# Performance work log

Measured on AMD Instinct MI355X. Metric: run time of the kernel, lower is better.

The kernel has to match this reference:

```python
import jax, jax.numpy as jnp
import numpy as np

SCALE = 8
NUM_CLASSES = 15
IGNORE_THRES = 0.5
# anchors for scale=8 divided by scale
GRID_ANCHOR = jnp.array([[96.0 / 8, 230.0 / 8], [79.0 / 8, 186.0 / 8], [81.0 / 8, 133.0 / 8]], dtype=jnp.float32)  # [3,2]


def _bce_sum(p, t, mask):
    # torch BCELoss(reduction='sum') with log clamped at -100, restricted to mask
    lp = jnp.maximum(jnp.log(p), -100.0)
    ln = jnp.maximum(jnp.log(1.0 - p), -100.0)
    return jnp.sum(-(t * lp + (1.0 - t) * ln) * mask)


def setup_inputs() -> dict:
    key = jax.random.key(0)
    k1, k2, k3 = jax.random.split(key, 3)
    nB, nG = 128, 52
    x = jax.random.normal(k1, (nB, 3 * (NUM_CLASSES + 5), nG, nG), dtype=jnp.float32)
    boxes = jax.random.uniform(k2, (nB, 4), minval=0.1, maxval=0.6)  # cx,cy,w,h in (0,1)
    cls = jax.random.randint(k3, (nB, 1), 0, NUM_CLASSES).astype(jnp.float32)
    labels = jnp.concatenate([boxes, cls], axis=-1)  # [nB,5]
    return {"x": x, "labels": labels}


def reference(x, labels):
    nB, nG = x.shape[0], x.shape[2]
    pred = x.reshape(nB, 3, NUM_CLASSES + 5, nG, nG).transpose(0, 1, 3, 4, 2)  # [B,3,G,G,20]
    px = jax.nn.sigmoid(pred[..., 0])
    py = jax.nn.sigmoid(pred[..., 1])
    pw = pred[..., 2]
    ph = pred[..., 3]
    conf = jax.nn.sigmoid(pred[..., 4])
    cls = jax.nn.softmax(pred[..., 5:], axis=-1)
    pred_boxs = jnp.stack([px, py, pw, ph], axis=-1)  # [B,3,G,G,4]
    out = jnp.concatenate([
        pred_boxs.reshape(nB, -1, 4) * SCALE,
        conf.reshape(nB, -1, 1),
        cls.reshape(nB, -1, NUM_CLASSES),
    ], axis=-1)

    # ---- build_targets (vectorized; one target per image as in original loop) ----
    tb = labels[:, :4] * nG  # boxes in grid units [B,4]
    gx, gy, gw, gh = tb[:, 0], tb[:, 1], tb[:, 2], tb[:, 3]
    gi = gx.astype(jnp.int32)
    gj = gy.astype(jnp.int32)
    gcls = labels[:, 4].astype(jnp.int32)

    # wh-IoU anchors vs targets -> [3,B]
    aw, ah = GRID_ANCHOR[:, 0:1], GRID_ANCHOR[:, 1:2]
    inter_wh = jnp.minimum(aw, gw[None, :]) * jnp.minimum(ah, gh[None, :])
    ious = inter_wh / (aw * ah + 1e-16 + gw[None, :] * gh[None, :] - inter_wh)
    best_idx = jnp.argmax(ious, axis=0)  # [B]

    bidx = jnp.arange(nB)
    shape4 = (nB, 3, nG, nG)
    obj = jnp.zeros(shape4, jnp.float32).at[bidx, best_idx, gj, gi].set(1.0)

    noobj = jnp.ones(shape4, jnp.float32)
    arep = jnp.tile(jnp.arange(3), nB)
    brep = jnp.repeat(bidx, 3)
    jrep = jnp.repeat(gj, 3)
    irep = jnp.repeat(gi, 3)
    ign = (jnp.reshape(ious.T, (-1,)) > IGNORE_THRES).astype(jnp.float32)
    noobj = noobj.at[brep, arep, jrep, irep].mul(1.0 - ign)
    noobj = noobj.at[bidx, best_idx, gj, gi].set(0.0)

    gif = gi.astype(jnp.float32)
    gjf = gj.astype(jnp.float32)
    tx = jnp.zeros(shape4, jnp.float32).at[bidx, best_idx, gj, gi].set(gx - gif)
    ty = jnp.zeros(shape4, jnp.float32).at[bidx, best_idx, gj, gi].set(gy - gjf)
    tw = jnp.zeros(shape4, jnp.float32).at[bidx, best_idx, gj, gi].set(jnp.log(gw / GRID_ANCHOR[best_idx, 0] + 1e-16))
    th = jnp.zeros(shape4, jnp.float32).at[bidx, best_idx, gj, gi].set(jnp.log(gh / GRID_ANCHOR[best_idx, 1] + 1e-16))
    tcls = jnp.zeros(shape4 + (NUM_CLASSES,), jnp.float32).at[bidx, best_idx, gj, gi, gcls].set(1.0)

    # cls_mask: does argmax of predicted class at target cell match gt class
    pred_cls_at = cls[bidx, best_idx, gj, gi]  # [B,15]
    cls_hit = (jnp.argmax(pred_cls_at, axis=-1) == gcls).astype(jnp.float32)
    cls_mask = jnp.zeros(shape4, jnp.float32).at[bidx, best_idx, gj, gi].set(cls_hit)

    # iou between pred box at target cell and target box (cxcywh, +1 corner convention)
    pb = pred_boxs[bidx, best_idx, gj, gi]  # [B,4]
    b1x1, b1y1 = pb[:, 0] - pb[:, 2] / 2, pb[:, 1] - pb[:, 3] / 2
    b1x2, b1y2 = pb[:, 0] + pb[:, 2] / 2, pb[:, 1] + pb[:, 3] / 2
    b2x1, b2y1 = gx - gw / 2, gy - gh / 2
    b2x2, b2y2 = gx + gw / 2, gy + gh / 2
    iw = jnp.clip(jnp.minimum(b1x2, b2x2) - jnp.maximum(b1x1, b2x1) + 1, 0)
    ih = jnp.clip(jnp.minimum(b1y2, b2y2) - jnp.maximum(b1y1, b2y1) + 1, 0)
    inter = iw * ih
    a1 = (b1x2 - b1x1 + 1) * (b1y2 - b1y1 + 1)
    a2 = (b2x2 - b2x1 + 1) * (b2y2 - b2y1 + 1)
    iou_vec = inter / (a1 + a2 - inter + 1e-16)
    iou_scores = jnp.zeros(shape4, jnp.float32).at[bidx, best_idx, gj, gi].set(iou_vec)

    tconf = obj
    # ---- losses (boolean-mask indexing replaced by masked sums) ----
    loss_x = jnp.sum(jnp.abs(px - tx) * obj)
    loss_y = jnp.sum(jnp.abs(py - ty) * obj)
    loss_w = jnp.sum(jnp.abs(pw - tw) * obj)
    loss_h = jnp.sum(jnp.abs(ph - th) * obj)
    loss_conf = _bce_sum(conf, tconf, obj) + 100.0 * _bce_sum(conf, tconf, noobj)
    loss_cls = _bce_sum(cls, tcls, obj[..., None])
    loss = loss_x + loss_y + loss_w + loss_h + loss_conf + loss_cls
    return (loss, out)
```

## Files before the change

kernel.cpp:

```cpp
#include <hip/hip_runtime.h>
#include <math.h>

#define NB    128
#define NG    52
#define NGG   2704
#define NA    3
#define NCLS  15
#define NCH   20
#define NQ    8112
#define TOTAL 1038336
#define BLK   256
#define NBLK  (TOTAL/BLK)
#define WPB   (BLK/64)
#define FPW   (64*NCH)
#define NPART (NBLK*WPB)

typedef float f4 __attribute__((ext_vector_type(4)));

__global__ __launch_bounds__(BLK) void main_kernel(const float* __restrict__ x,
                                                   const float* __restrict__ labels,
                                                   float* __restrict__ out,
                                                   float* __restrict__ partials) {
    __shared__ __align__(16) float sm[WPB][FPW];

    int t = threadIdx.x;
    int w = t >> 6;
    int l = t & 63;
    int cell = blockIdx.x * BLK + t;
    int b  = cell / NQ;
    int r  = cell - b * NQ;
    int a  = r / NGG;
    int ji = r - a * NGG;

    const float* __restrict__ xp = x + ((size_t)(b*60 + a*20)) * NGG + ji;
    float z[NCH];
    #pragma unroll
    for (int c = 0; c < NCH; c++) z[c] = xp[c * NGG];

    float v[NCH];
    float conf = 1.0f / (1.0f + __expf(-z[4]));
    v[0] = 8.0f / (1.0f + __expf(-z[0]));
    v[1] = 8.0f / (1.0f + __expf(-z[1]));
    v[2] = 8.0f * z[2];
    v[3] = 8.0f * z[3];
    v[4] = conf;
    float m = z[5];
    #pragma unroll
    for (int c = 6; c < NCH; c++) m = fmaxf(m, z[c]);
    float s = 0.0f;
    #pragma unroll
    for (int c = 0; c < NCLS; c++) { v[5+c] = __expf(z[5+c] - m); s += v[5+c]; }
    float inv = 1.0f / s;
    #pragma unroll
    for (int c = 0; c < NCLS; c++) v[5+c] *= inv;

    float gx = labels[b*5+0] * (float)NG;
    float gy = labels[b*5+1] * (float)NG;
    float gw = labels[b*5+2] * (float)NG;
    float gh = labels[b*5+3] * (float)NG;
    int  gcls = (int)labels[b*5+4];
    int gi = (int)gx, gj = (int)gy;
    float gwgh = gw * gh;
    float i0 = fminf(12.0f,   gw) * fminf(28.75f,  gh);
    float i1 = fminf(9.875f,  gw) * fminf(23.25f,  gh);
    float i2 = fminf(10.125f, gw) * fminf(16.625f, gh);
    float iou0 = i0 / (345.0f      + 1e-16f + gwgh - i0);
    float iou1 = i1 / (229.59375f  + 1e-16f + gwgh - i1);
    float iou2 = i2 / (168.328125f + 1e-16f + gwgh - i2);
    int best = 0; float bv = iou0;
    if (iou1 > bv) { best = 1; bv = iou1; }
    if (iou2 > bv) { best = 2; bv = iou2; }
    float ioua = (a == 0) ? iou0 : ((a == 1) ? iou1 : iou2);
    bool at_t   = (ji == gj * NG + gi);
    bool isbest = (a == best);

    float tsum = 0.0f;
    if (!(at_t && (isbest || ioua > 0.5f)))
        tsum = -100.0f * fmaxf(__logf(1.0f - conf), -100.0f);
    if (at_t && isbest) {
        tsum += -fmaxf(__logf(conf), -100.0f);
        float txv = gx - (float)gi;
        float tyv = gy - (float)gj;
        float abw = (best == 0) ? 12.0f  : ((best == 1) ? 9.875f : 10.125f);
        float abh = (best == 0) ? 28.75f : ((best == 1) ? 23.25f : 16.625f);
        float twv = __logf(gw / abw + 1e-16f);
        float thv = __logf(gh / abh + 1e-16f);
        tsum += fabsf(v[0]*0.125f - txv) + fabsf(v[1]*0.125f - tyv)
              + fabsf(v[2]*0.125f - twv) + fabsf(v[3]*0.125f - thv);
        #pragma unroll
        for (int c = 0; c < NCLS; c++) {
            float p = v[5+c];
            tsum += (c == gcls) ? -fmaxf(__logf(p),        -100.0f)
                                : -fmaxf(__logf(1.0f - p), -100.0f);
        }
    }

    float* __restrict__ smw = sm[w];
    int base = l * NCH - 3;
    #pragma unroll
    for (int c = 0; c < NCH; c++) {
        int L = base + c;
        if (L < 0) L += FPW;
        smw[L] = v[c];
    }

    #pragma unroll
    for (int off = 32; off > 0; off >>= 1) tsum += __shfl_down(tsum, off, 64);

    int cell0 = blockIdx.x * BLK + w * 64;
    size_t gf = 1 + (size_t)cell0 * NCH;
    f4* __restrict__ op = (f4*)(out + gf + 3);
    const f4* __restrict__ sp = (const f4*)smw;
    #pragma unroll
    for (int k = 0; k < 5; k++) {
        int q = k * 64 + l;
        if (q < (FPW - 4) / 4) op[q] = sp[q];
    }
    if (l == 0) {
        out[gf + 0]       = smw[FPW - 3];
        out[gf + 1]       = smw[FPW - 2];
        out[gf + 2]       = smw[FPW - 1];
        out[gf + FPW - 1] = smw[FPW - 4];
        partials[blockIdx.x * WPB + w] = tsum;
    }
}

__global__ __launch_bounds__(1024) void finish_kernel(const float* __restrict__ partials,
                                                      float* __restrict__ out) {
    int t = threadIdx.x;
    float s = 0.0f;
    #pragma unroll
    for (int k = 0; k < NPART/1024 + 1; k++) {
        int q = k * 1024 + t;
        if (q < NPART) s += partials[q];
    }
    __shared__ float red[1024];
    red[t] = s;
    __syncthreads();
    for (int k = 512; k > 0; k >>= 1) {
        if (t < k) red[t] += red[t + k];
        __syncthreads();
    }
    if (t == 0) out[0] = red[0];
}

extern "C" void kernel_launch(void* const* d_in, const int* in_sizes, int n_in,
                              void* d_out, int out_size, void* d_ws, size_t ws_size,
                              hipStream_t stream) {
    const float* x      = (const float*)d_in[0];
    const float* labels = (const float*)d_in[1];
    float* out = (float*)d_out;
    float* ws  = (float*)d_ws;

    hipLaunchKernelGGL(main_kernel,   dim3(NBLK), dim3(BLK),  0, stream, x, labels, out, ws);
    hipLaunchKernelGGL(finish_kernel, dim3(1),    dim3(1024), 0, stream, ws, out);
}
```

Measured before the change: 152.5 us.

## Load inputs directly into LDS with plane-aligned wave mapping

Each wave now covers 64 consecutive cells of a single (batch, anchor) plane, with a partial last wave per plane. The 20 channel values are fetched with global_load_lds straight into shared memory and then read back per lane, instead of strided global loads into registers. The aim is to cut register staging and load latency, and to keep every wave's channel loads contiguous. In exchange, some lanes sit idle in the tail wave of each plane, and the output-store bounds logic gets more complex.

```diff
diff --git a/kernel.cpp b/kernel.cpp
--- a/kernel.cpp
+++ b/kernel.cpp
@@ -7,15 +7,23 @@
 #define NA    3
 #define NCLS  15
 #define NCH   20
-#define NQ    8112
 #define TOTAL 1038336
+#define PLANES (NB*NA)
+#define WVP   43
+#define NSLOT (PLANES*WVP)
+#define WPB   4
 #define BLK   256
-#define NBLK  (TOTAL/BLK)
-#define WPB   (BLK/64)
+#define NBLK2 (NSLOT/WPB)
 #define FPW   (64*NCH)
-#define NPART (NBLK*WPB)
+#define NPART NSLOT
 
 typedef float f4 __attribute__((ext_vector_type(4)));
+
+__device__ __forceinline__ void gload_lds(const float* g, float* l) {
+    __builtin_amdgcn_global_load_lds(
+        (const __attribute__((address_space(1))) void*)g,
+        (__attribute__((address_space(3))) void*)l, 4, 0, 0);
+}
 
 __global__ __launch_bounds__(BLK) void main_kernel(const float* __restrict__ x,
                                                    const float* __restrict__ labels,
@@ -26,16 +34,31 @@
     int t = threadIdx.x;
     int w = t >> 6;
     int l = t & 63;
-    int cell = blockIdx.x * BLK + t;
-    int b  = cell / NQ;
-    int r  = cell - b * NQ;
-    int a  = r / NGG;
-    int ji = r - a * NGG;
+    int wslot = blockIdx.x * WPB + w;
+    int p  = wslot / WVP;
+    int k  = wslot - p * WVP;
+    int b  = p / 3;
+    int a  = p - b * 3;
+    int ji0 = k * 64;
+    int ji  = ji0 + l;
+    bool active = (ji < NGG);
+    int NACT = (NGG - ji0 < 64) ? (NGG - ji0) : 64;
+    int FACT = NACT * NCH;
 
-    const float* __restrict__ xp = x + ((size_t)(b*60 + a*20)) * NGG + ji;
+    float* __restrict__ smw = sm[w];
+    const float* __restrict__ xplane = x + ((size_t)(b*60 + a*20)) * NGG + ji0;
+
+    if (active) {
+        #pragma unroll
+        for (int c = 0; c < NCH; c++)
+            gload_lds(xplane + c * NGG + l, &smw[c * 64]);
+    }
+    asm volatile("s_waitcnt vmcnt(0)" ::: "memory");
+    __builtin_amdgcn_sched_barrier(0);
+
     float z[NCH];
     #pragma unroll
-    for (int c = 0; c < NCH; c++) z[c] = xp[c * NGG];
+    for (int c = 0; c < NCH; c++) z[c] = smw[c * 64 + l];
 
     float v[NCH];
     float conf = 1.0f / (1.0f + __expf(-z[4]));
@@ -75,53 +98,58 @@
     bool isbest = (a == best);
 
     float tsum = 0.0f;
-    if (!(at_t && (isbest || ioua > 0.5f)))
-        tsum = -100.0f * fmaxf(__logf(1.0f - conf), -100.0f);
-    if (at_t && isbest) {
-        tsum += -fmaxf(__logf(conf), -100.0f);
-        float txv = gx - (float)gi;
-        float tyv = gy - (float)gj;
-        float abw = (best == 0) ? 12.0f  : ((best == 1) ? 9.875f : 10.125f);
-        float abh = (best == 0) ? 28.75f : ((best == 1) ? 23.25f : 16.625f);
-        float twv = __logf(gw / abw + 1e-16f);
-        float thv = __logf(gh / abh + 1e-16f);
-        tsum += fabsf(v[0]*0.125f - txv) + fabsf(v[1]*0.125f - tyv)
-              + fabsf(v[2]*0.125f - twv) + fabsf(v[3]*0.125f - thv);
-        #pragma unroll
-        for (int c = 0; c < NCLS; c++) {
-            float p = v[5+c];
-            tsum += (c == gcls) ? -fmaxf(__logf(p),        -100.0f)
-                                : -fmaxf(__logf(1.0f - p), -100.0f);
+    if (active) {
+        if (!(at_t && (isbest || ioua > 0.5f)))
+            tsum = -100.0f * fmaxf(__logf(1.0f - conf), -100.0f);
+        if (at_t && isbest) {
+            tsum += -fmaxf(__logf(conf), -100.0f);
+            float txv = gx - (float)gi;
+            float tyv = gy - (float)gj;
+            float abw = (best == 0) ? 12.0f  : ((best == 1) ? 9.875f : 10.125f);
+            float abh = (best == 0) ? 28.75f : ((best == 1) ? 23.25f : 16.625f);
+            float twv = __logf(gw / abw + 1e-16f);
+            float thv = __logf(gh / abh + 1e-16f);
+            tsum += fabsf(v[0]*0.125f - txv) + fabsf(v[1]*0.125f - tyv)
+                  + fabsf(v[2]*0.125f - twv) + fabsf(v[3]*0.125f - thv);
+            #pragma unroll
+            for (int c = 0; c < NCLS; c++) {
+                float pc = v[5+c];
+                tsum += (c == gcls) ? -fmaxf(__logf(pc),        -100.0f)
+                                    : -fmaxf(__logf(1.0f - pc), -100.0f);
+            }
         }
     }
 
-    float* __restrict__ smw = sm[w];
-    int base = l * NCH - 3;
-    #pragma unroll
-    for (int c = 0; c < NCH; c++) {
-        int L = base + c;
-        if (L < 0) L += FPW;
-        smw[L] = v[c];
+    asm volatile("s_waitcnt lgkmcnt(0)" ::: "memory");
+    if (active) {
+        int base = l * NCH - 3;
+        #pragma unroll
+        for (int c = 0; c < NCH; c++) {
+            int L = base + c;
+            if (L < 0) L += FPW;
+            smw[L] = v[c];
+        }
     }
 
     #pragma unroll
     for (int off = 32; off > 0; off >>= 1) tsum += __shfl_down(tsum, off, 64);
 
-    int cell0 = blockIdx.x * BLK + w * 64;
+    int NQ4w = (FACT - 4) / 4;
+    int cell0 = p * NGG + ji0;
     size_t gf = 1 + (size_t)cell0 * NCH;
     f4* __restrict__ op = (f4*)(out + gf + 3);
     const f4* __restrict__ sp = (const f4*)smw;
     #pragma unroll
-    for (int k = 0; k < 5; k++) {
-        int q = k * 64 + l;
-        if (q < (FPW - 4) / 4) op[q] = sp[q];
+    for (int kk = 0; kk < 5; kk++) {
+        int q = kk * 64 + l;
+        if (q < NQ4w) op[q] = sp[q];
     }
     if (l == 0) {
-        out[gf + 0]       = smw[FPW - 3];
-        out[gf + 1]       = smw[FPW - 2];
-        out[gf + 2]       = smw[FPW - 1];
-        out[gf + FPW - 1] = smw[FPW - 4];
-        partials[blockIdx.x * WPB + w] = tsum;
+        out[gf + 0]        = smw[FPW - 3];
+        out[gf + 1]        = smw[FPW - 2];
+        out[gf + 2]        = smw[FPW - 1];
+        out[gf + FACT - 1] = smw[FACT - 4];
+        partials[wslot] = tsum;
     }
 }
 
@@ -152,6 +180,6 @@
     float* out = (float*)d_out;
     float* ws  = (float*)d_ws;
 
-    hipLaunchKernelGGL(main_kernel,   dim3(NBLK), dim3(BLK),  0, stream, x, labels, out, ws);
-    hipLaunchKernelGGL(finish_kernel, dim3(1),    dim3(1024), 0, stream, ws, out);
+    hipLaunchKernelGGL(main_kernel,   dim3(NBLK2), dim3(BLK),  0, stream, x, labels, out, ws);
+    hipLaunchKernelGGL(finish_kernel, dim3(1),     dim3(1024), 0, stream, ws, out);
 }
```

Result: no change. 152.0 us (-0.3%).
